# Performance work log

Measured on AMD Instinct MI355X. Metric: run time of the kernel, lower is better.

Reference implementation:

```python
import math
import jax, jax.numpy as jnp
import numpy as np

C = 64
GRID = 2

def _conv1x1(x, W, b):
    # 1x1 conv == channel-mixing matmul: [B,C,H,W] x [O,C] -> [B,O,H,W]
    return jnp.einsum('bchw,oc->bohw', x, W) + b[None, :, None, None]

def setup_inputs() -> dict:
    key = jax.random.key(0)
    ks = jax.random.split(key, 11)
    s = 1.0 / math.sqrt(C)
    def w(k):
        return jax.random.normal(k, (C, C), dtype=jnp.float32) * s
    def bias(k):
        return jax.random.normal(k, (C,), dtype=jnp.float32) * 0.02
    return {
        'x': jax.random.normal(ks[0], (2, C, 128, 128), dtype=jnp.float32),
        'Wq': w(ks[1]), 'bq': bias(ks[2]),
        'Wk': w(ks[3]), 'bk': bias(ks[4]),
        'Wa': w(ks[5]), 'ba': bias(ks[6]),
        'Wb': w(ks[7]), 'bb': bias(ks[8]),
        'Wo': w(ks[9]), 'bo': bias(ks[10]),
    }

def reference(x, Wq, bq, Wk, bk, Wa, ba, Wb, bb, Wo, bo):
    B, c, H, W = x.shape
    g = GRID
    rh, rw = H // g, W // g  # H,W chosen divisible by grid -> no reflect pad
    N = rh * rw
    R = g * g

    q = _conv1x1(x, Wq, bq)
    k = _conv1x1(x, Wk, bk)
    a = _conv1x1(x, Wa, ba)
    bt = _conv1x1(x, Wb, bb)

    def regionize(t):
        # [B,C,H,W] -> [B, R, C, N] with N = rh*rw row-major per region
        return t.reshape(B, c, g, rh, g, rw).transpose(0, 2, 4, 1, 3, 5).reshape(B, R, c, N)

    qr, kr, ar, br = regionize(q), regionize(k), regionize(a), regionize(bt)

    # attn[b,r,n,m] = softmax_m( q^T k / sqrt(C) )
    attn = jax.nn.softmax(jnp.einsum('brcn,brcm->brnm', qr, kr) / math.sqrt(c), axis=-1)

    # out_r = alpha @ attn + beta @ attn^T
    out = (jnp.einsum('brcj,brjm->brcm', ar, attn)
           + jnp.einsum('brcj,brmj->brcm', br, attn))

    # [B,R,C,N] -> [B,C,H,W]
    out = out.reshape(B, g, g, c, rh, rw).transpose(0, 3, 1, 4, 2, 5).reshape(B, c, H, W)
    return _conv1x1(out, Wo, bo)
```

## Files before the change

### kernel.cpp

```cpp
#include <hip/hip_runtime.h>


typedef __attribute__((ext_vector_type(8)))  short bf16x8;
typedef __attribute__((ext_vector_type(16))) float f32x16;

#define MFMA32(a, b, c) __builtin_amdgcn_mfma_f32_32x32x16_bf16(a, b, c, 0, 0, 0)

constexpr int REG_ELEMS = 4096 * 64;
constexpr size_t QP_OFF    = 0;
constexpr size_t KP_OFF    = 4u  << 20;
constexpr size_t ATL_OFF   = 8u  << 20;
constexpr size_t BTL_OFF   = 12u << 20;
constexpr size_t OUTP_OFF  = 16u << 20;
constexpr size_t LNV_OFF   = 20u << 20;
constexpr size_t LPART_OFF = (20u << 20) + (128u << 10);

constexpr float QSCALE = 0.18033688011112042f;

__device__ __forceinline__ short f2bf(float f) {
    union { float f; unsigned u; } v; v.f = f;
    unsigned r = v.u + 0x7fffu + ((v.u >> 16) & 1u);
    return (short)(r >> 16);
}
__device__ __forceinline__ float bf2f(short s) {
    union { unsigned u; float f; } v; v.u = ((unsigned)(unsigned short)s) << 16;
    return v.f;
}
__device__ __forceinline__ unsigned fbits(float f) {
    union { float f; unsigned u; } v; v.f = f; return v.u;
}
__device__ __forceinline__ unsigned pack_trunc(float e0, float e1) {
    return __builtin_amdgcn_perm(fbits(e1), fbits(e0), 0x07060302u);
}
__device__ __forceinline__ f32x16 zero16() {
    f32x16 z;
    #pragma unroll
    for (int i = 0; i < 16; ++i) z[i] = 0.f;
    return z;
}
__device__ __forceinline__ float fexp2(float x) {
#if __has_builtin(__builtin_amdgcn_exp2f)
    return __builtin_amdgcn_exp2f(x);
#else
    return exp2f(x);
#endif
}
__device__ __forceinline__ void permswap32(unsigned& a, unsigned& b, bool hi) {
#if __has_builtin(__builtin_amdgcn_permlane32_swap)
    auto r = __builtin_amdgcn_permlane32_swap(a, b, false, false);
    a = r[0]; b = r[1];
#elif __has_builtin(__builtin_amdgcn_permlane32_swap_b32)
    auto r = __builtin_amdgcn_permlane32_swap_b32(a, b, false, false);
    a = r[0]; b = r[1];
#else
    unsigned ax = (unsigned)__shfl_xor((int)a, 32);
    unsigned bx = (unsigned)__shfl_xor((int)b, 32);
    unsigned na = hi ? bx : a;
    unsigned nb = hi ? b  : ax;
    a = na; b = nb;
#endif
}

typedef __attribute__((address_space(1))) const unsigned char as1_t;
typedef __attribute__((address_space(3))) unsigned char as3_t;
__device__ __forceinline__ void stage16(const void* g, void* l) {
    __builtin_amdgcn_global_load_lds((as1_t*)g, (as3_t*)l, 16, 0, 0);
}

__global__ __launch_bounds__(256) void k_conv_in(
    const float* __restrict__ x,
    const float* __restrict__ Wq, const float* __restrict__ bq,
    const float* __restrict__ Wk, const float* __restrict__ bk,
    const float* __restrict__ Wa, const float* __restrict__ ba,
    const float* __restrict__ Wb, const float* __restrict__ bb,
    char* __restrict__ ws)
{
    const int tid  = threadIdx.x;
    const int blk  = blockIdx.x;
    const int wseg = blk & 1;
    const int h    = (blk >> 1) & 127;
    const int b    = blk >> 8;
    const int br   = b * 4 + (h >> 6) * 2 + wseg;
    const int n0   = (h & 63) * 64;

    __shared__ float xs[64][68];
    __shared__ short trans[2][64][72];

    const float* xp = x + ((size_t)b * 64 * 16384) + (size_t)h * 128 + wseg * 64;
    #pragma unroll
    for (int r = 0; r < 4; ++r) {
        int idx = r * 256 + tid;
        int c   = idx >> 4;
        int w4  = (idx & 15) << 2;
        *(float4*)&xs[c][w4] = *(const float4*)(xp + (size_t)c * 16384 + w4);
    }
    __syncthreads();

    const int lane = tid & 63;
    const int wid  = tid >> 6;
    const int col  = lane & 31;
    const int l5   = lane >> 5;
    const int pH   = wid & 1;
    const int oH   = wid >> 1;
    const int px   = pH * 32 + col;
    const int oc   = oH * 32 + col;

    bf16x8 xhi[4], xlo[4];
    #pragma unroll
    for (int s = 0; s < 4; ++s) {
        union { bf16x8 v; short sh[8]; } uh, ul;
        #pragma unroll
        for (int e = 0; e < 8; ++e) {
            float xv = xs[s * 16 + l5 * 8 + e][px];
            short hh = f2bf(xv);
            uh.sh[e] = hh;
            ul.sh[e] = f2bf(xv - bf2f(hh));
        }
        xhi[s] = uh.v; xlo[s] = ul.v;
    }

    #pragma unroll
    for (int mat = 0; mat < 4; ++mat) {
        const float* Wsel = (mat == 0) ? Wq : (mat == 1) ? Wk : (mat == 2) ? Wa : Wb;
        const float* bsel = (mat == 0) ? bq : (mat == 1) ? bk : (mat == 2) ? ba : bb;

        bf16x8 whi[4], wlo[4];
        const float* wrow = Wsel + (size_t)oc * 64;
        #pragma unroll
        for (int s = 0; s < 4; ++s) {
            float4 f0 = *(const float4*)(wrow + s * 16 + l5 * 8);
            float4 f1 = *(const float4*)(wrow + s * 16 + l5 * 8 + 4);
            float wf[8] = { f0.x, f0.y, f0.z, f0.w, f1.x, f1.y, f1.z, f1.w };
            union { bf16x8 v; short sh[8]; } uh, ul;
            #pragma unroll
            for (int e = 0; e < 8; ++e) {
                short hh = f2bf(wf[e]);
                uh.sh[e] = hh;
                ul.sh[e] = f2bf(wf[e] - bf2f(hh));
            }
            whi[s] = uh.v; wlo[s] = ul.v;
        }

        f32x16 d = zero16();
        #pragma unroll
        for (int s = 0; s < 4; ++s) {
            d = MFMA32(xhi[s], whi[s], d);
            d = MFMA32(xhi[s], wlo[s], d);
            d = MFMA32(xlo[s], whi[s], d);
        }

        const float bias = bsel[oc];
        if (mat < 2) {
            const float sc = (mat == 0) ? QSCALE : 1.0f;
            #pragma unroll
            for (int r = 0; r < 16; ++r) {
                int pxl = pH * 32 + (r & 3) + 8 * (r >> 2) + 4 * l5;
                trans[mat][pxl][oc] = f2bf((d[r] + bias) * sc);
            }
        } else {
            short* base = (short*)(ws + (mat == 2 ? ATL_OFF : BTL_OFF))
                          + (size_t)br * REG_ELEMS;
            const int sw   = (oc >> 1) & 3;
            const int tile = (n0 >> 5) + pH;
            #pragma unroll
            for (int q = 0; q < 4; ++q) {
                short tmp4[4];
                #pragma unroll
                for (int rr = 0; rr < 4; ++rr) tmp4[rr] = f2bf(d[4 * q + rr] + bias);
                int segp = q ^ sw;
                short* p = base + (size_t)tile * 2048 + oc * 32 + segp * 8 + 4 * l5;
                *(uint2*)p = *(uint2*)tmp4;
            }
        }
    }
    __syncthreads();

    #pragma unroll
    for (int rep = 0; rep < 4; ++rep) {
        int idx  = rep * 256 + tid;
        int mat2 = idx >> 9;
        int row  = (idx >> 3) & 63;
        int seg  = idx & 7;
        short* dst = (short*)(ws + (mat2 ? KP_OFF : QP_OFF))
                     + (size_t)br * REG_ELEMS + (size_t)(n0 + row) * 64
                     + (seg ^ (row & 7)) * 8;
        *(uint4*)dst = *(uint4*)&trans[mat2][row][seg * 8];
    }
}

__global__ __launch_bounds__(256, 2) void k_stats(char* __restrict__ ws)
{
    const int tid  = threadIdx.x;
    const int br   = blockIdx.x & 7;
    const int nt   = (blockIdx.x >> 3) & 63;
    const int ms   = blockIdx.x >> 9;
    const int lane = tid & 63;
    const int w    = tid >> 6;
    const int wn   = w & 1;
    const int wi   = w >> 1;
    const int col  = lane & 31;
    const int l5   = lane >> 5;

    const short* Qb  = (const short*)(ws + QP_OFF) + (size_t)br * REG_ELEMS;
    const char*  Kbb = ws + KP_OFF + (size_t)br * REG_ELEMS * 2
                       + (size_t)ms * 262144;

    __shared__ __align__(16) char smem[16896];

    const int nrow = nt * 64 + wn * 32 + col;
    bf16x8 afr[4];
    #pragma unroll
    for (int s = 0; s < 4; ++s)
        afr[s] = *(const bf16x8*)(Qb + (size_t)nrow * 64 + (((2*s+l5) ^ (col & 7)) * 8));

    float sm[16];
    #pragma unroll
    for (int r = 0; r < 16; ++r) sm[r] = 0.f;

    {
        const char* g = Kbb + (size_t)w * 2048 + lane * 16;
        char* l = smem + w * 2048;
        stage16(g, l); stage16(g + 1024, l + 1024);
    }

    #pragma unroll 2
    for (int slab = 0; slab < 32; ++slab) {
        __syncthreads();
        if (slab + 1 < 32) {
            const char* g = Kbb + (size_t)(slab + 1) * 8192 + w * 2048 + lane * 16;
            char* l = smem + ((slab + 1) & 1) * 8192 + w * 2048;
            stage16(g, l); stage16(g + 1024, l + 1024);
        }
        const short* Ks = (const short*)(smem + (slab & 1) * 8192);
        f32x16 d = zero16();
        #pragma unroll
        for (int s = 0; s < 4; ++s) {
            bf16x8 bf = *(const bf16x8*)(Ks + (wi * 32 + col) * 64
                                         + ((2*s+l5) ^ (col & 7)) * 8);
            d = MFMA32(afr[s], bf, d);
        }
        #pragma unroll
        for (int r = 0; r < 16; ++r) sm[r] += fexp2(d[r]);
    }

    #pragma unroll
    for (int off = 1; off < 32; off <<= 1)
        #pragma unroll
        for (int r = 0; r < 16; ++r) sm[r] += __shfl_xor(sm[r], off);

    __syncthreads();
    float* Lred = (float*)(smem + 16384);
    if (col == 0) {
        #pragma unroll
        for (int r = 0; r < 16; ++r)
            Lred[w * 32 + ((r & 3) + 8 * (r >> 2) + 4 * l5)] = sm[r];
    }
    __syncthreads();
    if (tid < 64) {
        int wn2 = tid >> 5, nl = tid & 31;
        float L = Lred[wn2 * 32 + nl] + Lred[(wn2 + 2) * 32 + nl];
        ((float*)(ws + LPART_OFF))[(size_t)ms * 32768 + (size_t)br * 4096
                                   + nt * 64 + tid] = L;
    }
}

__global__ __launch_bounds__(256) void k_ascale(char* __restrict__ ws)
{
    const int tid = threadIdx.x;
    const int br  = blockIdx.x & 7;
    const int nt  = blockIdx.x >> 3;

    __shared__ float Larr[64];

    if (tid < 64) {
        const float* Lp = (const float*)(ws + LPART_OFF);
        const size_t idx = (size_t)br * 4096 + nt * 64 + tid;
        float li = 1.0f / (Lp[idx] + Lp[32768 + idx]);
        Larr[tid] = li;
        ((float*)(ws + LNV_OFF))[idx] = li;
    }
    __syncthreads();

    short* Ab = (short*)(ws + ATL_OFF) + (size_t)br * REG_ELEMS + (size_t)nt * 4096;
    #pragma unroll
    for (int rep = 0; rep < 2; ++rep) {
        int id = rep * 256 + tid;
        int t = id >> 8, c = (id >> 2) & 63, s = id & 3;
        int sg = s ^ ((c >> 1) & 3);
        int jl = t * 32 + sg * 8;
        short* p = Ab + (size_t)t * 2048 + c * 32 + s * 8;
        uint4 v = *(uint4*)p;
        short* sp = (short*)&v;
        short o[8];
        #pragma unroll
        for (int e = 0; e < 8; ++e) o[e] = f2bf(bf2f(sp[e]) * Larr[jl + e]);
        *(uint4*)p = *(uint4*)o;
    }
}

__global__ __launch_bounds__(512, 2) void k_attn(char* __restrict__ ws)
{
    const int tid  = threadIdx.x;
    const int br   = blockIdx.x & 7;
    const int mt   = blockIdx.x >> 3;
    const int lane = tid & 63;
    const int w    = tid >> 6;
    const int wj   = w & 1;
    const int jsw  = (w >> 1) & 1;
    const int mh   = w >> 2;
    const int col  = lane & 31;
    const int l5   = lane >> 5;
    const bool hi  = (l5 != 0);

    const char* Qbb = ws + QP_OFF  + (size_t)br * REG_ELEMS * 2;
    const char* Kbb = ws + KP_OFF  + (size_t)br * REG_ELEMS * 2;
    const char* Abb = ws + ATL_OFF + (size_t)br * REG_ELEMS * 2;
    const char* Bbb = ws + BTL_OFF + (size_t)br * REG_ELEMS * 2;
    const float* Lnv = (const float*)(ws + LNV_OFF) + (size_t)br * 4096;
    short* OutPb    = (short*)(ws + OUTP_OFF) + (size_t)br * REG_ELEMS;

    __shared__ __align__(16) char smem[65536];

    const short* msrcb = (const short*)(wj == 0 ? Kbb : Qbb);
    bf16x8 mf[2][4];
    #pragma unroll
    for (int h = 0; h < 2; ++h) {
        const short* mr = msrcb + (size_t)(mt * 128 + mh * 64 + h * 32 + col) * 64;
        #pragma unroll
        for (int s = 0; s < 4; ++s)
            mf[h][s] = *(const bf16x8*)(mr + ((2*s+l5) ^ (col & 7)) * 8);
    }

    f32x16 acc00 = zero16(), acc01 = zero16();
    f32x16 acc10 = zero16(), acc11 = zero16();

    const int tt = w & 3;
    const int hh = w >> 2;
    const char* gsb = (tt == 0) ? Qbb : (tt == 1) ? Kbb : (tt == 2) ? Abb : Bbb;

    {
        const char* g = gsb + (size_t)hh * 262144 + lane * 16;
        char* l = smem + hh * 16384 + tt * 4096 + lane * 16;
        #pragma unroll
        for (int i = 0; i < 4; ++i) stage16(g + i * 1024, l + i * 1024);
    }

    #pragma unroll 2
    for (int rnd = 0; rnd < 64; ++rnd) {
        __syncthreads();
        if (rnd + 1 < 64) {
            const char* g = gsb + (size_t)hh * 262144
                            + (size_t)(rnd + 1) * 4096 + lane * 16;
            char* l = smem + ((rnd + 1) & 1) * 32768 + hh * 16384
                      + tt * 4096 + lane * 16;
            #pragma unroll
            for (int i = 0; i < 4; ++i) stage16(g + i * 1024, l + i * 1024);
        }
        const char* sb = smem + (rnd & 1) * 32768 + jsw * 16384;
        const short* jr = (const short*)(sb + (wj == 0 ? 0 : 4096));
        const short* ts = (const short*)(sb + (wj == 0 ? 8192 : 12288));

        bf16x8 a[4];
        #pragma unroll
        for (int s = 0; s < 4; ++s)
            a[s] = *(const bf16x8*)(jr + col * 64 + ((2*s+l5) ^ (col & 7)) * 8);

        f32x16 d0 = zero16(), d1 = zero16();
        #pragma unroll
        for (int s = 0; s < 4; ++s) {
            d0 = MFMA32(a[s], mf[0][s], d0);
            d1 = MFMA32(a[s], mf[1][s], d1);
        }

        unsigned W0[8], W1[8];
        #pragma unroll
        for (int q = 0; q < 4; ++q) {
            W0[2*q]   = pack_trunc(fexp2(d0[4*q]),   fexp2(d0[4*q+1]));
            W0[2*q+1] = pack_trunc(fexp2(d0[4*q+2]), fexp2(d0[4*q+3]));
            W1[2*q]   = pack_trunc(fexp2(d1[4*q]),   fexp2(d1[4*q+1]));
            W1[2*q+1] = pack_trunc(fexp2(d1[4*q+2]), fexp2(d1[4*q+3]));
        }

        #pragma unroll
        for (int k16 = 0; k16 < 2; ++k16) {
            unsigned u0 = W0[4*k16+0], u1 = W0[4*k16+1];
            unsigned u2 = W0[4*k16+2], u3 = W0[4*k16+3];
            permswap32(u0, u2, hi);
            permswap32(u1, u3, hi);
            union { uint4 u; bf16x8 v; } fr0;
            fr0.u.x = u0; fr0.u.y = u1; fr0.u.z = u2; fr0.u.w = u3;

            unsigned v0 = W1[4*k16+0], v1 = W1[4*k16+1];
            unsigned v2 = W1[4*k16+2], v3 = W1[4*k16+3];
            permswap32(v0, v2, hi);
            permswap32(v1, v3, hi);
            union { uint4 u; bf16x8 v; } fr1;
            fr1.u.x = v0; fr1.u.y = v1; fr1.u.z = v2; fr1.u.w = v3;

            const int swz = ((2*k16 + l5) ^ ((col >> 1) & 3)) * 8;
            bf16x8 bL = *(const bf16x8*)(ts + col * 32 + swz);
            bf16x8 bH = *(const bf16x8*)(ts + (col + 32) * 32 + swz);
            acc00 = MFMA32(fr0.v, bL, acc00);
            acc01 = MFMA32(fr0.v, bH, acc01);
            acc10 = MFMA32(fr1.v, bL, acc10);
            acc11 = MFMA32(fr1.v, bH, acc11);
        }
    }

    __syncthreads();
    float* red = (float*)smem;
    const int low2 = w & 3;
    if (low2 == 0) {
        #pragma unroll
        for (int h = 0; h < 2; ++h)
            #pragma unroll
            for (int r = 0; r < 16; ++r) {
                int ml = mh * 64 + h * 32 + (r & 3) + 8 * (r >> 2) + 4 * l5;
                red[ml * 68 + col]      = h ? acc10[r] : acc00[r];
                red[ml * 68 + 32 + col] = h ? acc11[r] : acc01[r];
            }
    }
    __syncthreads();
    if (low2 == 2) {
        #pragma unroll
        for (int h = 0; h < 2; ++h)
            #pragma unroll
            for (int r = 0; r < 16; ++r) {
                int ml = mh * 64 + h * 32 + (r & 3) + 8 * (r >> 2) + 4 * l5;
                red[ml * 68 + col]      += h ? acc10[r] : acc00[r];
                red[ml * 68 + 32 + col] += h ? acc11[r] : acc01[r];
            }
    }
    __syncthreads();
    if (low2 == 1) {
        #pragma unroll
        for (int h = 0; h < 2; ++h)
            #pragma unroll
            for (int r = 0; r < 16; ++r) {
                int ml = mh * 64 + h * 32 + (r & 3) + 8 * (r >> 2) + 4 * l5;
                float li = Lnv[mt * 128 + ml];
                red[ml * 68 + col]      += li * (h ? acc10[r] : acc00[r]);
                red[ml * 68 + 32 + col] += li * (h ? acc11[r] : acc01[r]);
            }
    }
    __syncthreads();
    if (low2 == 3) {
        #pragma unroll
        for (int h = 0; h < 2; ++h)
            #pragma unroll
            for (int r = 0; r < 16; ++r) {
                int ml = mh * 64 + h * 32 + (r & 3) + 8 * (r >> 2) + 4 * l5;
                float li = Lnv[mt * 128 + ml];
                red[ml * 68 + col]      += li * (h ? acc10[r] : acc00[r]);
                red[ml * 68 + 32 + col] += li * (h ? acc11[r] : acc01[r]);
            }
    }
    __syncthreads();
    {
        const int m  = tid >> 2;
        const int c0 = (tid & 3) * 16;
        const float* rp = red + m * 68 + c0;
        uint4 p0, p1;
        p0.x = pack_trunc(rp[0],  rp[1]);  p0.y = pack_trunc(rp[2],  rp[3]);
        p0.z = pack_trunc(rp[4],  rp[5]);  p0.w = pack_trunc(rp[6],  rp[7]);
        p1.x = pack_trunc(rp[8],  rp[9]);  p1.y = pack_trunc(rp[10], rp[11]);
        p1.z = pack_trunc(rp[12], rp[13]); p1.w = pack_trunc(rp[14], rp[15]);
        short* orow = OutPb + (size_t)(mt * 128 + m) * 64 + c0;
        *(uint4*)orow       = p0;
        *(uint4*)(orow + 8) = p1;
    }
}

__global__ __launch_bounds__(256) void k_conv_out(
    const char* __restrict__ ws,
    const float* __restrict__ Wo, const float* __restrict__ bo,
    float* __restrict__ out)
{
    const int tid  = threadIdx.x;
    const int lane = tid & 63;
    const int sub  = tid >> 6;
    const int blk  = blockIdx.x;
    const int br   = blk & 7;
    const int nt   = (blk >> 3) * 4 + sub;
    const int col  = lane & 31;
    const int l5   = lane >> 5;

    const short* OutPb = (const short*)(ws + OUTP_OFF) + (size_t)br * REG_ELEMS;

    bf16x8 afr[4];
    const short* arow = OutPb + (size_t)(nt * 32 + col) * 64 + l5 * 8;
    #pragma unroll
    for (int s = 0; s < 4; ++s) afr[s] = *(const bf16x8*)(arow + s * 16);

    bf16x8 bw[2][4];
    #pragma unroll
    for (int oh = 0; oh < 2; ++oh) {
        const float* wrow = Wo + (size_t)(oh * 32 + col) * 64 + l5 * 8;
        #pragma unroll
        for (int s = 0; s < 4; ++s) {
            float4 f0 = *(const float4*)(wrow + s * 16);
            float4 f1 = *(const float4*)(wrow + s * 16 + 4);
            union { bf16x8 v; short sh[8]; } u;
            u.sh[0] = f2bf(f0.x); u.sh[1] = f2bf(f0.y);
            u.sh[2] = f2bf(f0.z); u.sh[3] = f2bf(f0.w);
            u.sh[4] = f2bf(f1.x); u.sh[5] = f2bf(f1.y);
            u.sh[6] = f2bf(f1.z); u.sh[7] = f2bf(f1.w);
            bw[oh][s] = u.v;
        }
    }

    f32x16 d0 = zero16(), d1 = zero16();
    #pragma unroll
    for (int s = 0; s < 4; ++s) {
        d0 = MFMA32(afr[s], bw[0][s], d0);
        d1 = MFMA32(afr[s], bw[1][s], d1);
    }

    const int b  = br >> 2;
    const int gi = (br >> 1) & 1;
    const int gj = br & 1;

    #pragma unroll
    for (int oh = 0; oh < 2; ++oh) {
        const int oc = oh * 32 + col;
        const float bias = bo[oc];
        const f32x16& d = oh ? d1 : d0;
        #pragma unroll
        for (int q = 0; q < 4; ++q) {
            int nloc = 8 * q + 4 * l5;
            int nreg = nt * 32 + nloc;
            int wp   = nreg & 63;
            int ip   = nreg >> 6;
            float4 v = make_float4(d[4*q+0] + bias, d[4*q+1] + bias,
                                   d[4*q+2] + bias, d[4*q+3] + bias);
            float* op = out + ((size_t)(b * 64 + oc)) * 16384
                        + (size_t)(gi * 64 + ip) * 128 + gj * 64 + wp;
            *(float4*)op = v;
        }
    }
}

extern "C" void kernel_launch(void* const* d_in, const int* in_sizes, int n_in,
                              void* d_out, int out_size, void* d_ws, size_t ws_size,
                              hipStream_t stream)
{
    const float* x  = (const float*)d_in[0];
    const float* Wq = (const float*)d_in[1];
    const float* bq = (const float*)d_in[2];
    const float* Wk = (const float*)d_in[3];
    const float* bk = (const float*)d_in[4];
    const float* Wa = (const float*)d_in[5];
    const float* ba = (const float*)d_in[6];
    const float* Wb = (const float*)d_in[7];
    const float* bb = (const float*)d_in[8];
    const float* Wo = (const float*)d_in[9];
    const float* bo = (const float*)d_in[10];
    char* ws   = (char*)d_ws;
    float* out = (float*)d_out;

    hipLaunchKernelGGL(k_conv_in,  dim3(512),  dim3(256), 0, stream,
                       x, Wq, bq, Wk, bk, Wa, ba, Wb, bb, ws);
    hipLaunchKernelGGL(k_stats,    dim3(1024), dim3(256), 0, stream, ws);
    hipLaunchKernelGGL(k_ascale,   dim3(512),  dim3(256), 0, stream, ws);
    hipLaunchKernelGGL(k_attn,     dim3(256),  dim3(512), 0, stream, ws);
    hipLaunchKernelGGL(k_conv_out, dim3(256),  dim3(256), 0, stream,
                       ws, Wo, bo, out);
}
```

Baseline: 197.9 us.

## Triple-buffer LDS staging and software-pipeline score MFMAs one round ahead

Grows shared memory from two to three 32KB slabs so global-to-LDS staging runs two rounds ahead. The QK score MFMAs for the next round are computed before the exp/pack and PV MFMAs of the current round, which overlaps matrix work with transcendental work. It uses a raw s_waitcnt plus s_barrier in place of __syncthreads. The cost is more LDS (96KB per block, which may lower occupancy) and extra live registers for the next round's scores.

```diff
diff --git a/kernel.cpp b/kernel.cpp
--- a/kernel.cpp
+++ b/kernel.cpp
@@ -319,7 +319,7 @@
     const float* Lnv = (const float*)(ws + LNV_OFF) + (size_t)br * 4096;
     short* OutPb    = (short*)(ws + OUTP_OFF) + (size_t)br * REG_ELEMS;
 
-    __shared__ __align__(16) char smem[65536];
+    __shared__ __align__(16) char smem[98304];
 
     const short* msrcb = (const short*)(wj == 0 ? Kbb : Qbb);
     bf16x8 mf[2][4];
@@ -330,46 +330,66 @@
         for (int s = 0; s < 4; ++s)
             mf[h][s] = *(const bf16x8*)(mr + ((2*s+l5) ^ (col & 7)) * 8);
     }
-
-    f32x16 acc00 = zero16(), acc01 = zero16();
-    f32x16 acc10 = zero16(), acc11 = zero16();
 
     const int tt = w & 3;
     const int hh = w >> 2;
     const char* gsb = (tt == 0) ? Qbb : (tt == 1) ? Kbb : (tt == 2) ? Abb : Bbb;
 
+    auto stageRound = [&](char* slab, int rnd) {
+        const char* g = gsb + (size_t)hh * 262144 + (size_t)rnd * 4096 + lane * 16;
+        char* l = slab + hh * 16384 + tt * 4096 + lane * 16;
+        #pragma unroll
+        for (int i = 0; i < 4; ++i) stage16(g + i * 1024, l + i * 1024);
+    };
+
+    char* sA = smem;
+    char* sB = smem + 32768;
+    char* sC = smem + 65536;
+
+    stageRound(sA, 0);
+    stageRound(sB, 1);
+
+    const int jroff = jsw * 16384 + (wj == 0 ? 0 : 4096);
+    const int tsoff = jsw * 16384 + (wj == 0 ? 8192 : 12288);
+
+    asm volatile("s_waitcnt vmcnt(0)\n\ts_barrier" ::: "memory");
+
+    f32x16 d0, d1;
     {
-        const char* g = gsb + (size_t)hh * 262144 + lane * 16;
-        char* l = smem + hh * 16384 + tt * 4096 + lane * 16;
-        #pragma unroll
-        for (int i = 0; i < 4; ++i) stage16(g + i * 1024, l + i * 1024);
-    }
-
-    #pragma unroll 2
-    for (int rnd = 0; rnd < 64; ++rnd) {
-        __syncthreads();
-        if (rnd + 1 < 64) {
-            const char* g = gsb + (size_t)hh * 262144
-                            + (size_t)(rnd + 1) * 4096 + lane * 16;
-            char* l = smem + ((rnd + 1) & 1) * 32768 + hh * 16384
-                      + tt * 4096 + lane * 16;
-            #pragma unroll
-            for (int i = 0; i < 4; ++i) stage16(g + i * 1024, l + i * 1024);
-        }
-        const char* sb = smem + (rnd & 1) * 32768 + jsw * 16384;
-        const short* jr = (const short*)(sb + (wj == 0 ? 0 : 4096));
-        const short* ts = (const short*)(sb + (wj == 0 ? 8192 : 12288));
-
+        const short* jr = (const short*)(sA + jroff);
         bf16x8 a[4];
         #pragma unroll
         for (int s = 0; s < 4; ++s)
             a[s] = *(const bf16x8*)(jr + col * 64 + ((2*s+l5) ^ (col & 7)) * 8);
-
-        f32x16 d0 = zero16(), d1 = zero16();
+        d0 = zero16(); d1 = zero16();
         #pragma unroll
         for (int s = 0; s < 4; ++s) {
             d0 = MFMA32(a[s], mf[0][s], d0);
             d1 = MFMA32(a[s], mf[1][s], d1);
+        }
+    }
+
+    f32x16 acc00 = zero16(), acc01 = zero16();
+    f32x16 acc10 = zero16(), acc11 = zero16();
+
+    #pragma unroll 2
+    for (int rnd = 0; rnd < 64; ++rnd) {
+        asm volatile("s_waitcnt vmcnt(0)\n\ts_barrier" ::: "memory");
+        if (rnd + 2 < 64) stageRound(sC, rnd + 2);
+
+        f32x16 n0, n1;
+        if (rnd + 1 < 64) {
+            const short* jr = (const short*)(sB + jroff);
+            bf16x8 a[4];
+            #pragma unroll
+            for (int s = 0; s < 4; ++s)
+                a[s] = *(const bf16x8*)(jr + col * 64 + ((2*s+l5) ^ (col & 7)) * 8);
+            n0 = zero16(); n1 = zero16();
+            #pragma unroll
+            for (int s = 0; s < 4; ++s) {
+                n0 = MFMA32(a[s], mf[0][s], n0);
+                n1 = MFMA32(a[s], mf[1][s], n1);
+            }
         }
 
         unsigned W0[8], W1[8];
@@ -381,6 +401,7 @@
             W1[2*q+1] = pack_trunc(fexp2(d1[4*q+2]), fexp2(d1[4*q+3]));
         }
 
+        const short* ts = (const short*)(sA + tsoff);
         #pragma unroll
         for (int k16 = 0; k16 < 2; ++k16) {
             unsigned u0 = W0[4*k16+0], u1 = W0[4*k16+1];
@@ -405,6 +426,9 @@
             acc10 = MFMA32(fr1.v, bL, acc10);
             acc11 = MFMA32(fr1.v, bH, acc11);
         }
+
+        if (rnd + 1 < 64) { d0 = n0; d1 = n1; }
+        char* t = sA; sA = sB; sB = sC; sC = t;
     }
 
     __syncthreads();
```

New measurement: 194.1 us. No clear change (-1.9%).

## Split attention key dimension across two blocks with fp32 partials reduced in conv_out

Applied to the files above, without the earlier changes.

The attention kernel's j-loop is split in half across two blocks (split-K), doubling the grid from 256 to 512 blocks. Each half writes fp32 partial outputs to separate workspace buffers, and the output conv sums them before converting to bf16. This aims to fill more of the GPU's compute units, at the cost of more workspace traffic and an extra partial read in the final kernel. The launch bound's min-blocks hint is also raised from 2 to 4, which may force register pressure.

```diff
diff --git a/kernel.cpp b/kernel.cpp
--- a/kernel.cpp
+++ b/kernel.cpp
@@ -11,9 +11,10 @@
 constexpr size_t KP_OFF    = 4u  << 20;
 constexpr size_t ATL_OFF   = 8u  << 20;
 constexpr size_t BTL_OFF   = 12u << 20;
-constexpr size_t OUTP_OFF  = 16u << 20;
-constexpr size_t LNV_OFF   = 20u << 20;
-constexpr size_t LPART_OFF = (20u << 20) + (128u << 10);
+constexpr size_t P0_OFF    = 16u << 20;
+constexpr size_t P1_OFF    = 24u << 20;
+constexpr size_t LNV_OFF   = 32u << 20;
+constexpr size_t LPART_OFF = (32u << 20) + (128u << 10);
 
 constexpr float QSCALE = 0.18033688011112042f;
 
@@ -298,11 +299,12 @@
     }
 }
 
-__global__ __launch_bounds__(512, 2) void k_attn(char* __restrict__ ws)
+__global__ __launch_bounds__(512, 4) void k_attn(char* __restrict__ ws)
 {
     const int tid  = threadIdx.x;
     const int br   = blockIdx.x & 7;
-    const int mt   = blockIdx.x >> 3;
+    const int mt   = (blockIdx.x >> 3) & 31;
+    const int js   = blockIdx.x >> 8;
     const int lane = tid & 63;
     const int w    = tid >> 6;
     const int wj   = w & 1;
@@ -317,7 +319,7 @@
     const char* Abb = ws + ATL_OFF + (size_t)br * REG_ELEMS * 2;
     const char* Bbb = ws + BTL_OFF + (size_t)br * REG_ELEMS * 2;
     const float* Lnv = (const float*)(ws + LNV_OFF) + (size_t)br * 4096;
-    short* OutPb    = (short*)(ws + OUTP_OFF) + (size_t)br * REG_ELEMS;
+    float* Pp = (float*)(ws + (js ? P1_OFF : P0_OFF)) + (size_t)br * REG_ELEMS;
 
     __shared__ __align__(16) char smem[65536];
 
@@ -339,17 +341,17 @@
     const char* gsb = (tt == 0) ? Qbb : (tt == 1) ? Kbb : (tt == 2) ? Abb : Bbb;
 
     {
-        const char* g = gsb + (size_t)hh * 262144 + lane * 16;
+        const char* g = gsb + (size_t)hh * 262144 + (size_t)js * 131072 + lane * 16;
         char* l = smem + hh * 16384 + tt * 4096 + lane * 16;
         #pragma unroll
         for (int i = 0; i < 4; ++i) stage16(g + i * 1024, l + i * 1024);
     }
 
     #pragma unroll 2
-    for (int rnd = 0; rnd < 64; ++rnd) {
+    for (int rnd = 0; rnd < 32; ++rnd) {
         __syncthreads();
-        if (rnd + 1 < 64) {
-            const char* g = gsb + (size_t)hh * 262144
+        if (rnd + 1 < 32) {
+            const char* g = gsb + (size_t)hh * 262144 + (size_t)js * 131072
                             + (size_t)(rnd + 1) * 4096 + lane * 16;
             char* l = smem + ((rnd + 1) & 1) * 32768 + hh * 16384
                       + tt * 4096 + lane * 16;
@@ -460,14 +462,10 @@
         const int m  = tid >> 2;
         const int c0 = (tid & 3) * 16;
         const float* rp = red + m * 68 + c0;
-        uint4 p0, p1;
-        p0.x = pack_trunc(rp[0],  rp[1]);  p0.y = pack_trunc(rp[2],  rp[3]);
-        p0.z = pack_trunc(rp[4],  rp[5]);  p0.w = pack_trunc(rp[6],  rp[7]);
-        p1.x = pack_trunc(rp[8],  rp[9]);  p1.y = pack_trunc(rp[10], rp[11]);
-        p1.z = pack_trunc(rp[12], rp[13]); p1.w = pack_trunc(rp[14], rp[15]);
-        short* orow = OutPb + (size_t)(mt * 128 + m) * 64 + c0;
-        *(uint4*)orow       = p0;
-        *(uint4*)(orow + 8) = p1;
+        float* orow = Pp + (size_t)(mt * 128 + m) * 64 + c0;
+        #pragma unroll
+        for (int i = 0; i < 4; ++i)
+            *(float4*)(orow + i * 4) = *(const float4*)(rp + i * 4);
     }
 }
 
@@ -485,12 +483,24 @@
     const int col  = lane & 31;
     const int l5   = lane >> 5;
 
-    const short* OutPb = (const short*)(ws + OUTP_OFF) + (size_t)br * REG_ELEMS;
+    const float* Pa = (const float*)(ws + P0_OFF) + (size_t)br * REG_ELEMS;
+    const float* Pb = (const float*)(ws + P1_OFF) + (size_t)br * REG_ELEMS;
 
     bf16x8 afr[4];
-    const short* arow = OutPb + (size_t)(nt * 32 + col) * 64 + l5 * 8;
-    #pragma unroll
-    for (int s = 0; s < 4; ++s) afr[s] = *(const bf16x8*)(arow + s * 16);
+    const size_t roff = (size_t)(nt * 32 + col) * 64 + l5 * 8;
+    #pragma unroll
+    for (int s = 0; s < 4; ++s) {
+        float4 a0 = *(const float4*)(Pa + roff + s * 16);
+        float4 a1 = *(const float4*)(Pa + roff + s * 16 + 4);
+        float4 b0 = *(const float4*)(Pb + roff + s * 16);
+        float4 b1 = *(const float4*)(Pb + roff + s * 16 + 4);
+        union { bf16x8 v; short sh[8]; } u;
+        u.sh[0] = f2bf(a0.x + b0.x); u.sh[1] = f2bf(a0.y + b0.y);
+        u.sh[2] = f2bf(a0.z + b0.z); u.sh[3] = f2bf(a0.w + b0.w);
+        u.sh[4] = f2bf(a1.x + b1.x); u.sh[5] = f2bf(a1.y + b1.y);
+        u.sh[6] = f2bf(a1.z + b1.z); u.sh[7] = f2bf(a1.w + b1.w);
+        afr[s] = u.v;
+    }
 
     bf16x8 bw[2][4];
     #pragma unroll
@@ -562,7 +572,7 @@
                        x, Wq, bq, Wk, bk, Wa, ba, Wb, bb, ws);
     hipLaunchKernelGGL(k_stats,    dim3(1024), dim3(256), 0, stream, ws);
     hipLaunchKernelGGL(k_ascale,   dim3(512),  dim3(256), 0, stream, ws);
-    hipLaunchKernelGGL(k_attn,     dim3(256),  dim3(512), 0, stream, ws);
+    hipLaunchKernelGGL(k_attn,     dim3(512),  dim3(512), 0, stream, ws);
     hipLaunchKernelGGL(k_conv_out, dim3(256),  dim3(256), 0, stream,
                        ws, Wo, bo, out);
 }
```

Measured after the change: 329.6 us. 1.67x slower.
